# Kernel optimization log

Measured on AMD Instinct MI355X. Metric: run time of the kernel, lower is better.

## Reference

```python
import jax, jax.numpy as jnp
import numpy as np

N_NODES = 100000
N_EDGES = 1600000
N_FEAT = 64
EXP_FEAT = 50
CUTOFF = 5.0
LOG2 = float(np.log(2.0))


def ssp(x):
    # ShiftedSoftplus: softplus(x) - log(2)
    return jax.nn.softplus(x) - LOG2


def setup_inputs() -> dict:
    key = jax.random.key(0)
    ks = jax.random.split(key, 16)
    s = 1.0 / np.sqrt(N_FEAT)
    se = 1.0 / np.sqrt(EXP_FEAT)
    return {
        "neighbour_index": jax.random.randint(ks[0], (2, N_EDGES), 0, N_NODES, dtype=jnp.int64)
        if jax.config.read("jax_enable_x64") else jax.random.randint(ks[0], (2, N_EDGES), 0, N_NODES, dtype=jnp.int32),
        "neighbour_distances": jax.random.uniform(ks[1], (N_EDGES,), jnp.float32) * CUTOFF,
        "node_features": jax.random.normal(ks[2], (N_NODES, N_FEAT), jnp.float32),
        # initial linear transform
        "lin_w": jax.random.uniform(ks[3], (N_FEAT, N_FEAT), jnp.float32, -s, s),
        "lin_b": jax.random.uniform(ks[4], (N_FEAT,), jnp.float32, -s, s),
        # filter MLP: [EXP_FEAT -> N_FEAT -> N_FEAT], ssp between layers
        "f_w1": jax.random.uniform(ks[5], (N_FEAT, EXP_FEAT), jnp.float32, -se, se),
        "f_b1": jax.random.uniform(ks[6], (N_FEAT,), jnp.float32, -se, se),
        "f_w2": jax.random.uniform(ks[7], (N_FEAT, N_FEAT), jnp.float32, -s, s),
        "f_b2": jax.random.uniform(ks[8], (N_FEAT,), jnp.float32, -s, s),
        # output MLP: [N_FEAT -> N_FEAT -> N_FEAT]
        "m_w1": jax.random.uniform(ks[9], (N_FEAT, N_FEAT), jnp.float32, -s, s),
        "m_b1": jax.random.uniform(ks[10], (N_FEAT,), jnp.float32, -s, s),
        "m_w2": jax.random.uniform(ks[11], (N_FEAT, N_FEAT), jnp.float32, -s, s),
        "m_b2": jax.random.uniform(ks[12], (N_FEAT,), jnp.float32, -s, s),
    }


def reference(neighbour_index, neighbour_distances, node_features,
              lin_w, lin_b, f_w1, f_b1, f_w2, f_b2,
              m_w1, m_b1, m_w2, m_b2):
    n_nodes = node_features.shape[0]
    src = neighbour_index[0]  # j (messages gathered from)
    dst = neighbour_index[1]  # i (messages aggregated into)

    # h_i <- W x_i
    h = node_features @ lin_w.T + lin_b  # [N, F]

    # Gaussian smearing of distances: [E, K]
    centers = jnp.linspace(0.0, CUTOFF, EXP_FEAT, dtype=node_features.dtype)
    delta = centers[1] - centers[0]
    coeff = -0.5 / (delta * delta)
    rbf = jnp.exp(coeff * (neighbour_distances[:, None] - centers[None, :]) ** 2)

    # filter MLP F(r_ij): [E, F]
    filt = ssp(rbf @ f_w1.T + f_b1) @ f_w2.T + f_b2

    # message m_ij = h_j * F(r_ij); scatter-add into targets
    msg = h[src] * filt  # [E, F]
    agg = jax.ops.segment_sum(msg, dst, num_segments=n_nodes)  # [N, F]

    # output MLP
    return ssp(agg @ m_w1.T + m_b1) @ m_w2.T + m_b2
```

## Files before the change

kernel.cpp:

```cpp
#include <hip/hip_runtime.h>
#include <hip/hip_fp16.h>

#define NF 64
#define KEXP 50
#define TBL 16384
#define CUTF 5.0f
#define LOG2C 0.6931471805599453f
#define GRP 32
#define GSH 5
#define NSC 256
#define GMAX 4096
#define SCAP 768
#define RPT (SCAP / 256)

typedef unsigned long long ull;
typedef _Float16 f16x8 __attribute__((ext_vector_type(8)));
typedef float f32x4 __attribute__((ext_vector_type(4)));

__device__ __forceinline__ float sspf(float x) {
    return fmaxf(x, 0.0f) + log1pf(expf(-fabsf(x))) - LOG2C;
}

__device__ __forceinline__ f16x8 load_wfrag(const float* __restrict__ w, int f, int k0) {
    const float4 q0 = *(const float4*)(w + (size_t)f * NF + k0);
    const float4 q1 = *(const float4*)(w + (size_t)f * NF + k0 + 4);
    f16x8 r;
    r[0] = (_Float16)q0.x; r[1] = (_Float16)q0.y; r[2] = (_Float16)q0.z; r[3] = (_Float16)q0.w;
    r[4] = (_Float16)q1.x; r[5] = (_Float16)q1.y; r[6] = (_Float16)q1.z; r[7] = (_Float16)q1.w;
    return r;
}

__device__ __forceinline__ f16x8 load_afrag_f32(const float* __restrict__ p) {
    const float4 q0 = *(const float4*)(p);
    const float4 q1 = *(const float4*)(p + 4);
    f16x8 r;
    r[0] = (_Float16)q0.x; r[1] = (_Float16)q0.y; r[2] = (_Float16)q0.z; r[3] = (_Float16)q0.w;
    r[4] = (_Float16)q1.x; r[5] = (_Float16)q1.y; r[6] = (_Float16)q1.z; r[7] = (_Float16)q1.w;
    return r;
}

__global__ void __launch_bounds__(256) build_tabnn_k(
    const float* __restrict__ f_w1, const float* __restrict__ f_b1,
    const float* __restrict__ f_w2, const float* __restrict__ f_b2,
    __half* __restrict__ tabnn) {
    const int tid = threadIdx.x;
    const int lane = tid & 63;
    const int wid = tid >> 6;
    float w1r[KEXP], w2r[NF];
    for (int k = 0; k < KEXP; ++k) w1r[k] = f_w1[lane * KEXP + k];
    for (int k = 0; k < NF; ++k)  w2r[k] = f_w2[lane * NF + k];
    const float b1 = f_b1[lane], b2 = f_b2[lane];
    const float delta = CUTF / (float)(KEXP - 1);
    const float coeff = -0.5f / (delta * delta);
    const float dstep = CUTF / (float)(TBL - 1);
    for (int tt = 0; tt < 16; ++tt) {
        const int t = blockIdx.x * 64 + wid * 16 + tt;
        const float d = (float)t * dstep;
        float rbfv = 0.f;
        if (lane < KEXP) {
            const float dd = d - (float)lane * delta;
            rbfv = expf(coeff * dd * dd);
        }
        float t1 = b1;
        for (int k = 0; k < KEXP; ++k) t1 = fmaf(__shfl(rbfv, k), w1r[k], t1);
        const float sv = sspf(t1);
        float t2 = b2;
        for (int k = 0; k < NF; ++k) t2 = fmaf(__shfl(sv, k), w2r[k], t2);
        tabnn[(size_t)t * NF + lane] = __float2half(t2);
    }
}

__global__ void __launch_bounds__(256) prep_k(
    const float* __restrict__ x, const float* __restrict__ w, const float* __restrict__ b,
    __half* __restrict__ h16, int n_nodes)
{
    __shared__ _Float16 stile[4][16][72];
    const int tid = threadIdx.x;
    const int lane = tid & 63;
    const int wid = tid >> 6;
    const int col = lane & 15;
    const int quad = lane >> 4;

    f16x8 bw[4][2];
    float bv[4];
    #pragma unroll
    for (int t = 0; t < 4; ++t) {
        #pragma unroll
        for (int kb = 0; kb < 2; ++kb)
            bw[t][kb] = load_wfrag(w, 16 * t + col, kb * 32 + quad * 8);
        bv[t] = b[16 * t + col];
    }

    const int ntiles = (n_nodes + 15) >> 4;
    for (int tile = blockIdx.x * 4 + wid; tile < ntiles; tile += gridDim.x * 4) {
        const int n0 = tile << 4;
        const int nr = min(n0 + col, n_nodes - 1);
        f16x8 a[2];
        #pragma unroll
        for (int kb = 0; kb < 2; ++kb)
            a[kb] = load_afrag_f32(x + (size_t)nr * NF + kb * 32 + quad * 8);
        f32x4 acc[4];
        #pragma unroll
        for (int t = 0; t < 4; ++t) acc[t] = (f32x4){bv[t], bv[t], bv[t], bv[t]};
        #pragma unroll
        for (int t = 0; t < 4; ++t)
            #pragma unroll
            for (int kb = 0; kb < 2; ++kb)
                acc[t] = __builtin_amdgcn_mfma_f32_16x16x32_f16(a[kb], bw[t][kb], acc[t], 0, 0, 0);
        #pragma unroll
        for (int t = 0; t < 4; ++t)
            #pragma unroll
            for (int r = 0; r < 4; ++r)
                stile[wid][quad * 4 + r][16 * t + col] = (_Float16)acc[t][r];
        __threadfence_block();
        #pragma unroll
        for (int it = 0; it < 2; ++it) {
            const int chunk = it * 64 + lane;
            const int row = chunk >> 3;
            const int off = (chunk & 7) * 8;
            const int n = n0 + row;
            if (n < n_nodes)
                *(uint4*)(h16 + (size_t)n * NF + off) = *(const uint4*)&stile[wid][row][off];
        }
        __threadfence_block();
    }
}

__global__ void __launch_bounds__(1024) hist_k(const int* __restrict__ nbr_dst,
                                               int n_edges, int ngroups, int chk,
                                               unsigned* __restrict__ cnt) {
    __shared__ unsigned cnt_s[GMAX];
    const int tid = threadIdx.x;
    const int c = blockIdx.x;
    const int e0 = c * chk;
    const int e1 = min(e0 + chk, n_edges);
    const int m = max(e1 - e0, 0);
    for (int g = tid; g < ngroups; g += 1024) cnt_s[g] = 0u;
    __syncthreads();
    for (int i = tid; i < m; i += 1024)
        atomicAdd(&cnt_s[(unsigned)nbr_dst[e0 + i] >> GSH], 1u);
    __syncthreads();
    const size_t ob = (size_t)c * ngroups;
    for (int g = tid; g < ngroups; g += 1024) cnt[ob + g] = cnt_s[g];
}

__global__ void __launch_bounds__(64) colscan_k(const unsigned* __restrict__ cnt,
                                                unsigned* __restrict__ colpre,
                                                unsigned* __restrict__ tot, int ngroups) {
    const int g = blockIdx.x;
    const int lane = threadIdx.x;
    unsigned v[4];
    unsigned s = 0u;
    #pragma unroll
    for (int j = 0; j < 4; ++j) {
        v[j] = cnt[(size_t)(4 * lane + j) * ngroups + g];
        s += v[j];
    }
    unsigned run = s;
    #pragma unroll
    for (int d = 1; d < 64; d <<= 1) {
        const unsigned t = __shfl_up(run, d, 64);
        if (lane >= d) run += t;
    }
    unsigned pre = run - s;
    #pragma unroll
    for (int j = 0; j < 4; ++j) {
        colpre[(size_t)(4 * lane + j) * ngroups + g] = pre;
        pre += v[j];
    }
    if (lane == 63) tot[g] = run;
}

__global__ void __launch_bounds__(64) base_k(const unsigned* __restrict__ tot,
                                             unsigned* __restrict__ gbase, int ngroups) {
    const int lane = threadIdx.x;
    unsigned carry = 0u;
    for (int base = 0; base < ngroups; base += 64) {
        const int g = base + lane;
        const unsigned v = (g < ngroups) ? tot[g] : 0u;
        unsigned run = v;
        #pragma unroll
        for (int d = 1; d < 64; d <<= 1) {
            const unsigned t = __shfl_up(run, d, 64);
            if (lane >= d) run += t;
        }
        if (g < ngroups) gbase[g] = carry + run - v;
        carry += (unsigned)__shfl((int)run, 63, 64);
    }
    if (lane == 0) gbase[ngroups] = carry;
}

__global__ void __launch_bounds__(1024) scatter2_k(const int* __restrict__ nbr,
                                                   const float* __restrict__ dist,
                                                   int n_edges, int ngroups, int chk,
                                                   const unsigned* __restrict__ colpre,
                                                   const unsigned* __restrict__ gbase,
                                                   ull* __restrict__ payload) {
    __shared__ unsigned cur_s[GMAX];
    const int tid = threadIdx.x;
    const int c = blockIdx.x;
    const int e0 = c * chk;
    const int e1 = min(e0 + chk, n_edges);
    const int m = max(e1 - e0, 0);
    const size_t ob = (size_t)c * ngroups;
    for (int g = tid; g < ngroups; g += 1024) cur_s[g] = gbase[g] + colpre[ob + g];
    __syncthreads();
    const float scale = (float)(TBL - 1) / CUTF;
    for (int i = tid; i < m; i += 1024) {
        const int e = e0 + i;
        const unsigned dst = (unsigned)nbr[n_edges + e];
        const unsigned src = (unsigned)nbr[e];
        const float xx = dist[e] * scale + 0.5f;
        int i0 = (int)xx;
        i0 = max(0, min(i0, TBL - 1));
        const ull rec = (ull)((unsigned)i0 << 7) |
                        ((ull)((src << 7) | (dst & (GRP - 1u))) << 32);
        const unsigned pos = atomicAdd(&cur_s[dst >> GSH], 1u);
        payload[pos] = rec;
    }
}

__global__ void __launch_bounds__(256) agg_k(
    const ull* __restrict__ payload, const unsigned* __restrict__ gbase,
    const __half* __restrict__ h16, const __half* __restrict__ tabnn,
    float* __restrict__ agg, int n_nodes)
{
    __shared__ ull sorted_s[SCAP];
    __shared__ unsigned cnt_s[GRP];
    __shared__ unsigned base_s[GRP];
    __shared__ unsigned cur_s[GRP];
    const int tid = threadIdx.x;
    const int lane = tid & 63;
    const int wid = tid >> 6;
    const int g = blockIdx.x;
    const unsigned beg = gbase[g];
    const unsigned end = gbase[g + 1];
    const unsigned tot = min(end - beg, (unsigned)SCAP);

    if (tid < GRP) cnt_s[tid] = 0u;
    __syncthreads();
    ull rec[RPT];
    #pragma unroll
    for (int k = 0; k < RPT; ++k) {
        const unsigned i = (unsigned)(k * 256) + tid;
        rec[k] = 0ull;
        if (i < tot) {
            rec[k] = payload[beg + i];
            atomicAdd(&cnt_s[(unsigned)(rec[k] >> 32) & (GRP - 1u)], 1u);
        }
    }
    __syncthreads();
    if (tid < GRP) {
        const unsigned c = cnt_s[tid];
        unsigned run = c;
        #pragma unroll
        for (int d = 1; d < GRP; d <<= 1) {
            const unsigned t = __shfl_up(run, d, 64);
            if (tid >= d) run += t;
        }
        base_s[tid] = run - c;
        cur_s[tid]  = run - c;
    }
    __syncthreads();
    #pragma unroll
    for (int k = 0; k < RPT; ++k) {
        const unsigned i = (unsigned)(k * 256) + tid;
        if (i < tot) {
            const unsigned pos = atomicAdd(&cur_s[(unsigned)(rec[k] >> 32) & (GRP - 1u)], 1u);
            sorted_s[pos] = rec[k];
        }
    }
    __syncthreads();
    const char* tabB = (const char*)tabnn + (lane << 1);
    const char* hB   = (const char*)h16 + (lane << 1);
    auto ev = [&](ull r) -> float {
        const unsigned lo = (unsigned)r;
        const unsigned hi = (unsigned)(r >> 32);
        const float tv = __half2float(*(const __half*)(tabB + lo));
        const float hv = __half2float(*(const __half*)(hB + (hi & 0xFFFFFF80u)));
        return tv * hv;
    };
    const int n0 = g * GRP;
    for (int rr = 0; rr < GRP / 4; ++rr) {
        const int r = wid * (GRP / 4) + rr;
        unsigned i = base_s[r];
        const unsigned e = cur_s[r];
        float acc0 = 0.f, acc1 = 0.f;
        for (; i + 16u <= e; i += 16u) {
            ull rv[16];
            #pragma unroll
            for (int j = 0; j < 16; ++j) rv[j] = sorted_s[i + j];
            float p[16];
            #pragma unroll
            for (int j = 0; j < 16; ++j) p[j] = ev(rv[j]);
            acc0 += ((p[0] + p[1]) + (p[2] + p[3])) + ((p[4] + p[5]) + (p[6] + p[7]));
            acc1 += ((p[8] + p[9]) + (p[10] + p[11])) + ((p[12] + p[13]) + (p[14] + p[15]));
        }
        for (; i + 4u <= e; i += 4u) {
            const ull r0 = sorted_s[i];
            const ull r1 = sorted_s[i + 1];
            const ull r2 = sorted_s[i + 2];
            const ull r3 = sorted_s[i + 3];
            acc0 += ev(r0) + ev(r1);
            acc1 += ev(r2) + ev(r3);
        }
        for (; i < e; ++i) acc0 += ev(sorted_s[i]);
        const int n = n0 + r;
        if (n < n_nodes) agg[(size_t)n * NF + lane] = acc0 + acc1;
    }
}

__global__ void __launch_bounds__(64) oflow2_k(const ull* __restrict__ payload,
                                               const unsigned* __restrict__ gbase,
                                               const __half* __restrict__ h16,
                                               const __half* __restrict__ tabnn,
                                               float* __restrict__ agg) {
    const int g = blockIdx.x;
    const unsigned beg = gbase[g];
    const unsigned end = gbase[g + 1];
    if (end - beg <= (unsigned)SCAP) return;
    const int lane = threadIdx.x;
    const char* tabB = (const char*)tabnn + (lane << 1);
    const char* hB   = (const char*)h16 + (lane << 1);
    for (unsigned i = beg + SCAP; i < end; ++i) {
        const ull rec = payload[i];
        const unsigned lo = (unsigned)rec;
        const unsigned hi = (unsigned)(rec >> 32);
        const float tv = __half2float(*(const __half*)(tabB + lo));
        const float hv = __half2float(*(const __half*)(hB + (hi & 0xFFFFFF80u)));
        const unsigned row = (unsigned)g * GRP + (hi & (GRP - 1u));
        atomicAdd(agg + (size_t)row * NF + lane, tv * hv);
    }
}

__global__ void edge_k(const int* __restrict__ nbr, const float* __restrict__ dist,
                       const __half* __restrict__ h16, const __half* __restrict__ tabnn,
                       float* __restrict__ agg, int n_edges) {
    const int tid = threadIdx.x;
    const int lane = tid & 63;
    const int nwaves = (gridDim.x * blockDim.x) >> 6;
    const int gw = (blockIdx.x * blockDim.x + tid) >> 6;
    const float scale = (float)(TBL - 1) / CUTF;
    const int nbatch = n_edges >> 6;
    for (int bb = gw; bb < nbatch; bb += nwaves) {
        const int e0 = bb << 6;
        int src = nbr[e0 + lane];
        int dst = nbr[n_edges + e0 + lane];
        float d = dist[e0 + lane];
        float xx = d * scale + 0.5f;
        int i0 = (int)xx;
        i0 = max(0, min(i0, TBL - 1));
        #pragma unroll 4
        for (int j = 0; j < 64; ++j) {
            const int sj = __shfl(src, j);
            const int dj = __shfl(dst, j);
            const int ij = __shfl(i0, j);
            const float tv = __half2float(tabnn[(size_t)ij * NF + lane]);
            const float hv = __half2float(h16[(size_t)sj * NF + lane]);
            atomicAdd(agg + (size_t)dj * NF + lane, tv * hv);
        }
    }
    if (gw == 0) {
        for (int e = nbatch << 6; e < n_edges; ++e) {
            const int sj = nbr[e];
            const int dj = nbr[n_edges + e];
            const float d = dist[e];
            float xx = d * scale + 0.5f;
            int ij = (int)xx;
            ij = max(0, min(ij, TBL - 1));
            const float tv = __half2float(tabnn[(size_t)ij * NF + lane]);
            const float hv = __half2float(h16[(size_t)sj * NF + lane]);
            atomicAdd(agg + (size_t)dj * NF + lane, tv * hv);
        }
    }
}

__global__ void __launch_bounds__(256) out_mlp_k(const float* __restrict__ agg,
                                                 const float* __restrict__ w1,
                                                 const float* __restrict__ b1,
                                                 const float* __restrict__ w2,
                                                 const float* __restrict__ b2,
                                                 float* __restrict__ out, int n_nodes) {
    __shared__ _Float16 stile[4][16][72];
    const int tid = threadIdx.x;
    const int lane = tid & 63;
    const int wid = tid >> 6;
    const int col = lane & 15;
    const int quad = lane >> 4;

    f16x8 bw1[4][2], bw2[4][2];
    float b1v[4], b2v[4];
    #pragma unroll
    for (int t = 0; t < 4; ++t) {
        #pragma unroll
        for (int kb = 0; kb < 2; ++kb) {
            bw1[t][kb] = load_wfrag(w1, 16 * t + col, kb * 32 + quad * 8);
            bw2[t][kb] = load_wfrag(w2, 16 * t + col, kb * 32 + quad * 8);
        }
        b1v[t] = b1[16 * t + col];
        b2v[t] = b2[16 * t + col];
    }

    const int ntiles = (n_nodes + 15) >> 4;
    for (int tile = blockIdx.x * 4 + wid; tile < ntiles; tile += gridDim.x * 4) {
        const int n0 = tile << 4;
        const int nr = min(n0 + col, n_nodes - 1);
        f16x8 a[2];
        #pragma unroll
        for (int kb = 0; kb < 2; ++kb)
            a[kb] = load_afrag_f32(agg + (size_t)nr * NF + kb * 32 + quad * 8);
        f32x4 acc[4];
        #pragma unroll
        for (int t = 0; t < 4; ++t) acc[t] = (f32x4){b1v[t], b1v[t], b1v[t], b1v[t]};
        #pragma unroll
        for (int t = 0; t < 4; ++t)
            #pragma unroll
            for (int kb = 0; kb < 2; ++kb)
                acc[t] = __builtin_amdgcn_mfma_f32_16x16x32_f16(a[kb], bw1[t][kb], acc[t], 0, 0, 0);
        #pragma unroll
        for (int t = 0; t < 4; ++t)
            #pragma unroll
            for (int r = 0; r < 4; ++r)
                stile[wid][quad * 4 + r][16 * t + col] = (_Float16)sspf(acc[t][r]);
        __threadfence_block();
        f16x8 a2[2];
        #pragma unroll
        for (int kb = 0; kb < 2; ++kb)
            a2[kb] = *(const f16x8*)&stile[wid][col][kb * 32 + quad * 8];
        f32x4 acc2[4];
        #pragma unroll
        for (int t = 0; t < 4; ++t) acc2[t] = (f32x4){b2v[t], b2v[t], b2v[t], b2v[t]};
        #pragma unroll
        for (int t = 0; t < 4; ++t)
            #pragma unroll
            for (int kb = 0; kb < 2; ++kb)
                acc2[t] = __builtin_amdgcn_mfma_f32_16x16x32_f16(a2[kb], bw2[t][kb], acc2[t], 0, 0, 0);
        #pragma unroll
        for (int t = 0; t < 4; ++t)
            #pragma unroll
            for (int r = 0; r < 4; ++r) {
                const int n = n0 + quad * 4 + r;
                if (n < n_nodes) out[(size_t)n * NF + 16 * t + col] = acc2[t][r];
            }
        __threadfence_block();
    }
}

extern "C" void kernel_launch(void* const* d_in, const int* in_sizes, int n_in,
                              void* d_out, int out_size, void* d_ws, size_t ws_size,
                              hipStream_t stream) {
    const int*   nbr   = (const int*)d_in[0];
    const float* dist  = (const float*)d_in[1];
    const float* x     = (const float*)d_in[2];
    const float* lin_w = (const float*)d_in[3];
    const float* lin_b = (const float*)d_in[4];
    const float* f_w1  = (const float*)d_in[5];
    const float* f_b1  = (const float*)d_in[6];
    const float* f_w2  = (const float*)d_in[7];
    const float* f_b2  = (const float*)d_in[8];
    const float* m_w1  = (const float*)d_in[9];
    const float* m_b1  = (const float*)d_in[10];
    const float* m_w2  = (const float*)d_in[11];
    const float* m_b2  = (const float*)d_in[12];

    const int n_edges = in_sizes[1];
    const int n_nodes = in_sizes[2] / NF;
    const int ngroups = (n_nodes + GRP - 1) / GRP;
    const int chk     = (n_edges + NSC - 1) / NSC;
    const int ntiles  = (n_nodes + 15) / 16;
    const int mlp_blk = (ntiles + 3) / 4;

    float* out = (float*)d_out;
    float* agg = out;

    char* ws = (char*)d_ws;
    size_t off = 0;
    auto alloc = [&](size_t bytes) { char* p = ws + off; off = (off + bytes + 255) & ~(size_t)255; return p; };
    __half*   h16     = (__half*)alloc((size_t)n_nodes * NF * sizeof(__half));
    __half*   tabnn   = (__half*)alloc((size_t)TBL * NF * sizeof(__half));
    unsigned* cnt     = (unsigned*)alloc((size_t)NSC * ngroups * sizeof(unsigned));
    unsigned* colpre  = (unsigned*)alloc((size_t)NSC * ngroups * sizeof(unsigned));
    unsigned* tot     = (unsigned*)alloc((size_t)ngroups * sizeof(unsigned));
    unsigned* gbase   = (unsigned*)alloc((size_t)(ngroups + 1) * sizeof(unsigned));
    ull*      payload = (ull*)alloc((size_t)NSC * chk * sizeof(ull));
    const bool sort_path = (off <= ws_size) && (ngroups <= GMAX) && (n_nodes <= (1 << 17));

    build_tabnn_k<<<TBL / 64, 256, 0, stream>>>(f_w1, f_b1, f_w2, f_b2, tabnn);
    prep_k<<<mlp_blk, 256, 0, stream>>>(x, lin_w, lin_b, h16, n_nodes);

    if (sort_path) {
        hist_k<<<NSC, 1024, 0, stream>>>(nbr + n_edges, n_edges, ngroups, chk, cnt);
        colscan_k<<<ngroups, 64, 0, stream>>>(cnt, colpre, tot, ngroups);
        base_k<<<1, 64, 0, stream>>>(tot, gbase, ngroups);
        scatter2_k<<<NSC, 1024, 0, stream>>>(nbr, dist, n_edges, ngroups, chk,
                                             colpre, gbase, payload);
        agg_k<<<ngroups, 256, 0, stream>>>(payload, gbase, h16, tabnn, agg, n_nodes);
        oflow2_k<<<ngroups, 64, 0, stream>>>(payload, gbase, h16, tabnn, agg);
    } else {
        hipMemsetAsync(agg, 0, (size_t)n_nodes * NF * sizeof(float), stream);
        edge_k<<<2048, 256, 0, stream>>>(nbr, dist, h16, tabnn, agg, n_edges);
    }
    out_mlp_k<<<mlp_blk, 256, 0, stream>>>(agg, m_w1, m_b1, m_w2, m_b2, out, n_nodes);
}
```

Before: 209.5 us.

## Merge table build, histogram and node transform into one heterogeneous launch

Folds the filter-table build, the destination histogram and the node linear transform into a single kernel, with each block picking its role by block index, so three launches become one and the independent stages can share the GPU at the same time. The histogram blocks drop from 1024 to 256 threads to fit the shared launch size. The softplus and RBF exponentials now use fast intrinsics, with slightly lower accuracy. The histogram always runs, even when the fallback path is taken, where it is unused.

```diff
diff --git a/kernel.cpp b/kernel.cpp
--- a/kernel.cpp
+++ b/kernel.cpp
@@ -4,6 +4,7 @@
 #define NF 64
 #define KEXP 50
 #define TBL 16384
+#define TBLBLK (TBL / 64)
 #define CUTF 5.0f
 #define LOG2C 0.6931471805599453f
 #define GRP 32
@@ -18,7 +19,7 @@
 typedef float f32x4 __attribute__((ext_vector_type(4)));
 
 __device__ __forceinline__ float sspf(float x) {
-    return fmaxf(x, 0.0f) + log1pf(expf(-fabsf(x))) - LOG2C;
+    return fmaxf(x, 0.0f) + __logf(1.0f + __expf(-fabsf(x))) - LOG2C;
 }
 
 __device__ __forceinline__ f16x8 load_wfrag(const float* __restrict__ w, int f, int k0) {
@@ -39,109 +40,106 @@
     return r;
 }
 
-__global__ void __launch_bounds__(256) build_tabnn_k(
+__global__ void __launch_bounds__(256) front_k(
     const float* __restrict__ f_w1, const float* __restrict__ f_b1,
     const float* __restrict__ f_w2, const float* __restrict__ f_b2,
-    __half* __restrict__ tabnn) {
+    __half* __restrict__ tabnn,
+    const int* __restrict__ nbr_dst, int n_edges, int ngroups, int chk,
+    unsigned* __restrict__ cnt,
+    const float* __restrict__ x, const float* __restrict__ w,
+    const float* __restrict__ b, __half* __restrict__ h16, int n_nodes)
+{
+    __shared__ __align__(16) char smem[GMAX * 4];
+    const int blk = blockIdx.x;
     const int tid = threadIdx.x;
     const int lane = tid & 63;
     const int wid = tid >> 6;
-    float w1r[KEXP], w2r[NF];
-    for (int k = 0; k < KEXP; ++k) w1r[k] = f_w1[lane * KEXP + k];
-    for (int k = 0; k < NF; ++k)  w2r[k] = f_w2[lane * NF + k];
-    const float b1 = f_b1[lane], b2 = f_b2[lane];
-    const float delta = CUTF / (float)(KEXP - 1);
-    const float coeff = -0.5f / (delta * delta);
-    const float dstep = CUTF / (float)(TBL - 1);
-    for (int tt = 0; tt < 16; ++tt) {
-        const int t = blockIdx.x * 64 + wid * 16 + tt;
-        const float d = (float)t * dstep;
-        float rbfv = 0.f;
-        if (lane < KEXP) {
-            const float dd = d - (float)lane * delta;
-            rbfv = expf(coeff * dd * dd);
-        }
-        float t1 = b1;
-        for (int k = 0; k < KEXP; ++k) t1 = fmaf(__shfl(rbfv, k), w1r[k], t1);
-        const float sv = sspf(t1);
-        float t2 = b2;
-        for (int k = 0; k < NF; ++k) t2 = fmaf(__shfl(sv, k), w2r[k], t2);
-        tabnn[(size_t)t * NF + lane] = __float2half(t2);
-    }
-}
-
-__global__ void __launch_bounds__(256) prep_k(
-    const float* __restrict__ x, const float* __restrict__ w, const float* __restrict__ b,
-    __half* __restrict__ h16, int n_nodes)
-{
-    __shared__ _Float16 stile[4][16][72];
-    const int tid = threadIdx.x;
-    const int lane = tid & 63;
-    const int wid = tid >> 6;
-    const int col = lane & 15;
-    const int quad = lane >> 4;
-
-    f16x8 bw[4][2];
-    float bv[4];
-    #pragma unroll
-    for (int t = 0; t < 4; ++t) {
-        #pragma unroll
-        for (int kb = 0; kb < 2; ++kb)
-            bw[t][kb] = load_wfrag(w, 16 * t + col, kb * 32 + quad * 8);
-        bv[t] = b[16 * t + col];
-    }
-
-    const int ntiles = (n_nodes + 15) >> 4;
-    for (int tile = blockIdx.x * 4 + wid; tile < ntiles; tile += gridDim.x * 4) {
-        const int n0 = tile << 4;
-        const int nr = min(n0 + col, n_nodes - 1);
-        f16x8 a[2];
-        #pragma unroll
-        for (int kb = 0; kb < 2; ++kb)
-            a[kb] = load_afrag_f32(x + (size_t)nr * NF + kb * 32 + quad * 8);
-        f32x4 acc[4];
-        #pragma unroll
-        for (int t = 0; t < 4; ++t) acc[t] = (f32x4){bv[t], bv[t], bv[t], bv[t]};
-        #pragma unroll
-        for (int t = 0; t < 4; ++t)
+
+    if (blk < TBLBLK) {
+        float w1r[KEXP], w2r[NF];
+        for (int k = 0; k < KEXP; ++k) w1r[k] = f_w1[lane * KEXP + k];
+        for (int k = 0; k < NF; ++k)  w2r[k] = f_w2[lane * NF + k];
+        const float b1 = f_b1[lane], b2 = f_b2[lane];
+        const float delta = CUTF / (float)(KEXP - 1);
+        const float coeff = -0.5f / (delta * delta);
+        const float dstep = CUTF / (float)(TBL - 1);
+        for (int tt = 0; tt < 16; ++tt) {
+            const int t = blk * 64 + wid * 16 + tt;
+            const float d = (float)t * dstep;
+            float rbfv = 0.f;
+            if (lane < KEXP) {
+                const float dd = d - (float)lane * delta;
+                rbfv = __expf(coeff * dd * dd);
+            }
+            float t1 = b1;
+            for (int k = 0; k < KEXP; ++k) t1 = fmaf(__shfl(rbfv, k), w1r[k], t1);
+            const float sv = sspf(t1);
+            float t2 = b2;
+            for (int k = 0; k < NF; ++k) t2 = fmaf(__shfl(sv, k), w2r[k], t2);
+            tabnn[(size_t)t * NF + lane] = __float2half(t2);
+        }
+    } else if (blk < TBLBLK + NSC) {
+        unsigned* cnt_s = (unsigned*)smem;
+        const int c = blk - TBLBLK;
+        const int e0 = c * chk;
+        const int e1 = min(e0 + chk, n_edges);
+        const int m = max(e1 - e0, 0);
+        for (int g = tid; g < ngroups; g += 256) cnt_s[g] = 0u;
+        __syncthreads();
+        for (int i = tid; i < m; i += 256)
+            atomicAdd(&cnt_s[(unsigned)nbr_dst[e0 + i] >> GSH], 1u);
+        __syncthreads();
+        const size_t ob = (size_t)c * ngroups;
+        for (int g = tid; g < ngroups; g += 256) cnt[ob + g] = cnt_s[g];
+    } else {
+        _Float16 (*stile)[16][72] = (_Float16(*)[16][72])smem;
+        const int col = lane & 15;
+        const int quad = lane >> 4;
+        f16x8 bw[4][2];
+        float bv[4];
+        #pragma unroll
+        for (int t = 0; t < 4; ++t) {
             #pragma unroll
             for (int kb = 0; kb < 2; ++kb)
-                acc[t] = __builtin_amdgcn_mfma_f32_16x16x32_f16(a[kb], bw[t][kb], acc[t], 0, 0, 0);
-        #pragma unroll
-        for (int t = 0; t < 4; ++t)
-            #pragma unroll
-            for (int r = 0; r < 4; ++r)
-                stile[wid][quad * 4 + r][16 * t + col] = (_Float16)acc[t][r];
-        __threadfence_block();
-        #pragma unroll
-        for (int it = 0; it < 2; ++it) {
-            const int chunk = it * 64 + lane;
-            const int row = chunk >> 3;
-            const int off = (chunk & 7) * 8;
-            const int n = n0 + row;
-            if (n < n_nodes)
-                *(uint4*)(h16 + (size_t)n * NF + off) = *(const uint4*)&stile[wid][row][off];
-        }
-        __threadfence_block();
-    }
-}
-
-__global__ void __launch_bounds__(1024) hist_k(const int* __restrict__ nbr_dst,
-                                               int n_edges, int ngroups, int chk,
-                                               unsigned* __restrict__ cnt) {
-    __shared__ unsigned cnt_s[GMAX];
-    const int tid = threadIdx.x;
-    const int c = blockIdx.x;
-    const int e0 = c * chk;
-    const int e1 = min(e0 + chk, n_edges);
-    const int m = max(e1 - e0, 0);
-    for (int g = tid; g < ngroups; g += 1024) cnt_s[g] = 0u;
-    __syncthreads();
-    for (int i = tid; i < m; i += 1024)
-        atomicAdd(&cnt_s[(unsigned)nbr_dst[e0 + i] >> GSH], 1u);
-    __syncthreads();
-    const size_t ob = (size_t)c * ngroups;
-    for (int g = tid; g < ngroups; g += 1024) cnt[ob + g] = cnt_s[g];
+                bw[t][kb] = load_wfrag(w, 16 * t + col, kb * 32 + quad * 8);
+            bv[t] = b[16 * t + col];
+        }
+        const int pb = blk - (TBLBLK + NSC);
+        const int pgrid = gridDim.x - (TBLBLK + NSC);
+        const int ntiles = (n_nodes + 15) >> 4;
+        for (int tile = pb * 4 + wid; tile < ntiles; tile += pgrid * 4) {
+            const int n0 = tile << 4;
+            const int nr = min(n0 + col, n_nodes - 1);
+            f16x8 a[2];
+            #pragma unroll
+            for (int kb = 0; kb < 2; ++kb)
+                a[kb] = load_afrag_f32(x + (size_t)nr * NF + kb * 32 + quad * 8);
+            f32x4 acc[4];
+            #pragma unroll
+            for (int t = 0; t < 4; ++t) acc[t] = (f32x4){bv[t], bv[t], bv[t], bv[t]};
+            #pragma unroll
+            for (int t = 0; t < 4; ++t)
+                #pragma unroll
+                for (int kb = 0; kb < 2; ++kb)
+                    acc[t] = __builtin_amdgcn_mfma_f32_16x16x32_f16(a[kb], bw[t][kb], acc[t], 0, 0, 0);
+            #pragma unroll
+            for (int t = 0; t < 4; ++t)
+                #pragma unroll
+                for (int r = 0; r < 4; ++r)
+                    stile[wid][quad * 4 + r][16 * t + col] = (_Float16)acc[t][r];
+            __threadfence_block();
+            #pragma unroll
+            for (int it = 0; it < 2; ++it) {
+                const int chunk = it * 64 + lane;
+                const int row = chunk >> 3;
+                const int off = (chunk & 7) * 8;
+                const int n = n0 + row;
+                if (n < n_nodes)
+                    *(uint4*)(h16 + (size_t)n * NF + off) = *(const uint4*)&stile[wid][row][off];
+            }
+            __threadfence_block();
+        }
+    }
 }
 
 __global__ void __launch_bounds__(64) colscan_k(const unsigned* __restrict__ cnt,
@@ -485,11 +483,12 @@
     ull*      payload = (ull*)alloc((size_t)NSC * chk * sizeof(ull));
     const bool sort_path = (off <= ws_size) && (ngroups <= GMAX) && (n_nodes <= (1 << 17));
 
-    build_tabnn_k<<<TBL / 64, 256, 0, stream>>>(f_w1, f_b1, f_w2, f_b2, tabnn);
-    prep_k<<<mlp_blk, 256, 0, stream>>>(x, lin_w, lin_b, h16, n_nodes);
+    front_k<<<TBLBLK + NSC + mlp_blk, 256, 0, stream>>>(
+        f_w1, f_b1, f_w2, f_b2, tabnn,
+        nbr + n_edges, n_edges, ngroups, chk, cnt,
+        x, lin_w, lin_b, h16, n_nodes);
 
     if (sort_path) {
-        hist_k<<<NSC, 1024, 0, stream>>>(nbr + n_edges, n_edges, ngroups, chk, cnt);
         colscan_k<<<ngroups, 64, 0, stream>>>(cnt, colpre, tot, ngroups);
         base_k<<<1, 64, 0, stream>>>(tot, gbase, ngroups);
         scatter2_k<<<NSC, 1024, 0, stream>>>(nbr, dist, n_edges, ngroups, chk,
```

New measurement: 203.1 us. -3.1%, faster.
